# Kernel optimization log

Measured on AMD Instinct MI355X. Metric: run time of the kernel, lower is better.

## Reference

```python
import jax, jax.numpy as jnp
import numpy as np

B, N = 1, 768
CM, CP = 384, 128            # msa_channel (single repr), pair_channel
H, SQK, SV, PQK, PV = 12, 16, 16, 4, 8
NOUT = 384
NFIN = H * SV + H * PV * 4 + H * CP  # 2112
FP16_HUGE = 65504.0
DIST_EPS = 1e-8


def _quat_to_rot(q):
    # normalized quaternion [B,N,4] -> rotation matrix [B,N,3,3]
    q = q / jnp.sqrt(jnp.sum(q * q, axis=-1, keepdims=True))
    w, x, y, z = q[..., 0], q[..., 1], q[..., 2], q[..., 3]
    return jnp.stack([
        jnp.stack([1 - 2 * (y * y + z * z), 2 * (x * y - w * z), 2 * (x * z + w * y)], -1),
        jnp.stack([2 * (x * y + w * z), 1 - 2 * (x * x + z * z), 2 * (y * z - w * x)], -1),
        jnp.stack([2 * (x * z - w * y), 2 * (y * z + w * x), 1 - 2 * (x * x + y * y)], -1),
    ], -2)


def setup_inputs() -> dict:
    key = jax.random.key(0)
    ks = jax.random.split(key, 20)
    s = 0.02
    return {
        'inputs_1d': jax.random.normal(ks[0], (B, N, CM), jnp.float32),
        'inputs_2d': jax.random.normal(ks[1], (B, N, N, CP), jnp.float32),
        'mask': jnp.ones((B, N, 1), jnp.float32),
        'quat': jax.random.normal(ks[2], (B, N, 4), jnp.float32),
        'trans': jax.random.normal(ks[3], (B, N, 3), jnp.float32),
        'wq': jax.random.normal(ks[4], (CM, H * SQK), jnp.float32) * s,
        'bq': jnp.zeros((H * SQK,), jnp.float32),
        'wkv': jax.random.normal(ks[5], (CM, H * (SQK + SV)), jnp.float32) * s,
        'bkv': jnp.zeros((H * (SQK + SV),), jnp.float32),
        'wqp': jax.random.normal(ks[6], (CM, H * 3 * PQK), jnp.float32) * s,
        'bqp': jnp.zeros((H * 3 * PQK,), jnp.float32),
        'wkvp': jax.random.normal(ks[7], (CM, H * 3 * (PQK + PV)), jnp.float32) * s,
        'bkvp': jnp.zeros((H * 3 * (PQK + PV),), jnp.float32),
        'pw_raw': jnp.full((H,), 0.541323855, jnp.float32),
        'w2d': jax.random.normal(ks[8], (CP, H), jnp.float32) * s,
        'b2d': jnp.zeros((H,), jnp.float32),
        'wout': jax.random.normal(ks[9], (NFIN, NOUT), jnp.float32) * s,
        'bout': jnp.zeros((NOUT,), jnp.float32),
    }


def _ipa(inputs_1d, inputs_2d, mask, quat, trans,
         wq, bq, wkv, bkv, wqp, bqp, wkvp, bkvp, pw_raw, w2d, b2d, wout, bout):
    R = _quat_to_rot(quat)                      # [B,N,3,3]

    # --- scalar q/k/v ---
    q_s = (inputs_1d @ wq + bq).reshape(B, N, H, SQK)
    kv_s = (inputs_1d @ wkv + bkv).reshape(B, N, H, SQK + SV)
    k_s, v_s = kv_s[..., :SQK], kv_s[..., SQK:]

    # --- point q/k/v in global frame: R @ p_local + t ---
    qp = (inputs_1d @ wqp + bqp).reshape(B, N, 3, H * PQK)  # split order: x,y,z blocks
    qp_g = jnp.einsum('bnij,bnjp->bnip', R, qp) + trans[..., None]
    kvp = (inputs_1d @ wkvp + bkvp).reshape(B, N, 3, H * (PQK + PV))
    kvp_g = (jnp.einsum('bnij,bnjp->bnip', R, kvp) + trans[..., None]
             ).reshape(B, N, 3, H, PQK + PV)
    kp_g, vp_g = kvp_g[..., :PQK], kvp_g[..., PQK:]

    # --- attention weights ---
    scalar_w = (1.0 / (3.0 * SQK)) ** 0.5
    point_w = ((1.0 / (3.0 * PQK * 4.5)) ** 0.5) * jax.nn.softplus(pw_raw)  # [H]

    # point-distance logits: -0.5*w_h * sum_{xyz,p} (q-k)^2, via |q|^2+|k|^2-2qk
    q_pt = jnp.transpose(qp_g.reshape(B, N, 3, H, PQK), (0, 3, 1, 2, 4)).reshape(B, H, N, 3 * PQK)
    k_pt = jnp.transpose(kp_g, (0, 3, 1, 2, 4)).reshape(B, H, N, 3 * PQK)
    qq = jnp.sum(q_pt * q_pt, -1)               # [B,H,N]
    kk = jnp.sum(k_pt * k_pt, -1)
    cross = jnp.einsum('bhnd,bhmd->bhnm', q_pt, k_pt)
    attn_pt = -0.5 * point_w[None, :, None, None] * (
        qq[..., :, None] + kk[..., None, :] - 2.0 * cross)

    attn_sc = jnp.einsum('bnhd,bmhd->bhnm', q_s * scalar_w, k_s)
    a2d = jnp.transpose(inputs_2d @ w2d + b2d, (0, 3, 1, 2)) * (1.0 / 3.0) ** 0.5

    logits = attn_sc + attn_pt + a2d
    mask2d = mask * jnp.swapaxes(mask, -1, -2)  # [B,N,N]
    logits = logits - FP16_HUGE * (1.0 - mask2d[:, None])
    attn = jax.nn.softmax(logits, axis=-1)      # [B,H,N,N]

    # --- aggregation ---
    res_s = jnp.einsum('bhnm,bmhd->bnhd', attn, v_s).reshape(B, N, H * SV)
    v_pt = jnp.transpose(vp_g, (0, 3, 1, 2, 4)).reshape(B, H, N, 3 * PV)
    res_pt_g = jnp.einsum('bhnm,bhmd->bhnd', attn, v_pt).reshape(B, H, N, 3, PV)
    res_pt_g = jnp.transpose(res_pt_g, (0, 2, 3, 1, 4)).reshape(B, N, 3, H * PV)
    # invert point: R^T (g - t)
    res_pt_l = jnp.einsum('bnji,bnjp->bnip', R, res_pt_g - trans[..., None])  # [B,N,3,H*PV]
    pt_norm = jnp.sqrt(DIST_EPS + jnp.sum(res_pt_l * res_pt_l, axis=2))       # [B,N,H*PV]
    res_2d = jnp.einsum('bhnm,bnmc->bnhc', attn, inputs_2d).reshape(B, N, H * CP)

    final = jnp.concatenate(
        [res_s, res_pt_l[:, :, 0], res_pt_l[:, :, 1], res_pt_l[:, :, 2], pt_norm, res_2d], -1)
    return final @ wout + bout


def reference(inputs_1d, inputs_2d, mask, quat, trans,
              wq, bq, wkv, bkv, wqp, bqp, wkvp, bkvp, pw_raw, w2d, b2d, wout, bout):
    return _ipa(inputs_1d, inputs_2d, mask, quat, trans,
                wq, bq, wkv, bkv, wqp, bqp, wkvp, bkvp, pw_raw, w2d, b2d, wout, bout)
```

## Files before the change

### kernel.cpp

```cpp
#include <hip/hip_runtime.h>
#include <cstdint>
#include <cstddef>

static constexpr float SCALAR_W = 0.14433756729740643f;
static constexpr float PTW_C    = 0.13608276348795434f;
static constexpr float RSQRT3   = 0.5773502691896258f;
static constexpr float FP16HUGE = 65504.0f;

static constexpr size_t OFF_P    = 0;
static constexpr size_t OFF_R    = 884736;
static constexpr size_t OFF_QPG  = 891648;
static constexpr size_t OFF_KVPG = 1002240;
static constexpr size_t OFF_LG   = 1334016;
static constexpr size_t OFF_FIN  = 8633088;
static constexpr size_t OFF_VCAT = 10255104;
static constexpr size_t OFF_KST  = 10623744;
static constexpr size_t OFF_KPT  = 10771200;
static constexpr size_t WS_TOTAL = 10881792;

__global__ void k_sentinel(float* __restrict__ out, int nel, float val)
{
    const int i = blockIdx.x * 256 + threadIdx.x;
    if (i < nel) out[i] = val;
}

__global__ __launch_bounds__(256) void k_proj_all(const float* __restrict__ A,
    const float* __restrict__ wq,  const float* __restrict__ bq,
    const float* __restrict__ wkv, const float* __restrict__ bkv,
    const float* __restrict__ wqp, const float* __restrict__ bqp,
    const float* __restrict__ wkvp,const float* __restrict__ bkvp,
    float* __restrict__ P)
{
    const int z = blockIdx.z;
    const float* Bm; const float* bias; int ncols, colbase;
    switch (z) {
        case 0: Bm = wq;   bias = bq;   ncols = 192; colbase = 0;   break;
        case 1: Bm = wkv;  bias = bkv;  ncols = 384; colbase = 192; break;
        case 2: Bm = wqp;  bias = bqp;  ncols = 144; colbase = 576; break;
        default:Bm = wkvp; bias = bkvp; ncols = 432; colbase = 720; break;
    }
    if (blockIdx.x * 256 >= ncols) return;
    __shared__ float At[8][384];
    const int t = threadIdx.x;
    const int r0 = blockIdx.y * 8;
    const float4* A4 = reinterpret_cast<const float4*>(A + (size_t)r0 * 384);
    float4* At4 = reinterpret_cast<float4*>(&At[0][0]);
#pragma unroll
    for (int i = 0; i < 3; ++i) At4[t + 256 * i] = A4[t + 256 * i];
    __syncthreads();
    const int col = blockIdx.x * 256 + t;
    if (col >= ncols) return;
    float acc[8] = {0.f,0.f,0.f,0.f,0.f,0.f,0.f,0.f};
    const float* bp = Bm + col;
#pragma unroll 4
    for (int k = 0; k < 384; ++k) {
        const float b = bp[(size_t)k * ncols];
#pragma unroll
        for (int r = 0; r < 8; ++r) acc[r] += At[r][k] * b;
    }
    const float bb = bias[col];
#pragma unroll
    for (int r = 0; r < 8; ++r)
        P[(size_t)(r0 + r) * 1152 + colbase + col] = acc[r] + bb;
}

__global__ __launch_bounds__(256) void k_rmat(const float* __restrict__ quat,
    float* __restrict__ ws)
{
    const int o = blockIdx.x * 256 + threadIdx.x;
    if (o >= 768 * 9) return;
    const int n = o / 9, e = o - 9 * n;
    const float q0 = quat[n*4+0], q1 = quat[n*4+1], q2 = quat[n*4+2], q3 = quat[n*4+3];
    const float inv = 1.0f / sqrtf(q0*q0 + q1*q1 + q2*q2 + q3*q3);
    const float w = q0*inv, x = q1*inv, y = q2*inv, z = q3*inv;
    float R[9];
    R[0] = 1.f - 2.f*(y*y + z*z); R[1] = 2.f*(x*y - w*z); R[2] = 2.f*(x*z + w*y);
    R[3] = 2.f*(x*y + w*z); R[4] = 1.f - 2.f*(x*x + z*z); R[5] = 2.f*(y*z - w*x);
    R[6] = 2.f*(x*z - w*y); R[7] = 2.f*(y*z + w*x); R[8] = 1.f - 2.f*(x*x + y*y);
    ws[OFF_R + o] = R[e];
}

__global__ __launch_bounds__(256) void k_rigid(const float* __restrict__ trans,
    float* __restrict__ ws)
{
    const int o = blockIdx.x * 256 + threadIdx.x;
    if (o >= 768 * 576) return;
    const int n = o / 576, e = o - 576 * n;
    const float* R = ws + OFF_R + (size_t)n * 9;
    if (e < 144) {
        const int i = e / 48, p = e - 48 * i;
        const float* Pn = ws + OFF_P + (size_t)n * 1152 + 576;
        ws[OFF_QPG + (size_t)n*144 + e] =
            R[i*3+0]*Pn[p] + R[i*3+1]*Pn[48+p] + R[i*3+2]*Pn[96+p] + trans[n*3+i];
    } else {
        const int e2 = e - 144;
        const int i = e2 / 144, p = e2 - 144 * i;
        const float* Pn = ws + OFF_P + (size_t)n * 1152 + 720;
        ws[OFF_KVPG + (size_t)n*432 + e2] =
            R[i*3+0]*Pn[p] + R[i*3+1]*Pn[144+p] + R[i*3+2]*Pn[288+p] + trans[n*3+i];
    }
}

__global__ __launch_bounds__(256) void k_vcat(float* __restrict__ ws)
{
    const int o = blockIdx.x * 256 + threadIdx.x;
    if (o >= 768 * 480) return;
    const int m = o / 480, q = o - 480 * m;
    float v;
    if (q < 192) {
        const int h = q >> 4, d = q & 15;
        v = ws[OFF_P + (size_t)m*1152 + 192 + h*32 + 16 + d];
    } else {
        const int q2 = q - 192;
        const int i = q2 / 96, r = q2 - 96*i, h = r >> 3, c = r & 7;
        v = ws[OFF_KVPG + (size_t)m*432 + i*144 + h*12 + 4 + c];
    }
    ws[OFF_VCAT + o] = v;
}

__global__ __launch_bounds__(256) void k_kt(float* __restrict__ ws)
{
    const int o = blockIdx.x * 256 + threadIdx.x;
    if (o >= 768 * 336) return;
    const int m = o / 336, q = o - 336 * m;
    if (q < 192) {
        const int h = q >> 4, k = q & 15;
        ws[OFF_KST + (size_t)(h*16 + k)*768 + m] =
            ws[OFF_P + (size_t)m*1152 + 192 + h*32 + k];
    } else {
        const int d2 = q - 192;
        const int h = d2 / 12, d = d2 - 12 * h;
        const int i = d >> 2, a = d & 3;
        ws[OFF_KPT + (size_t)(h*12 + d)*768 + m] =
            ws[OFF_KVPG + (size_t)m*432 + i*144 + h*12 + a];
    }
}

__global__ __launch_bounds__(256) void k_lga(const float* __restrict__ in2d,
    const float* __restrict__ w2d, const float* __restrict__ b2d,
    const float* __restrict__ maskp, const float* __restrict__ pw_raw,
    float* __restrict__ ws)
{
    __shared__ float w2l[1536];
    __shared__ float a2l[12][132];
    __shared__ float qs[192], qpl[144], pwl[12], b2l[12];
    const int n = blockIdx.x, mt = blockIdx.y, t = threadIdx.x;
    if (t < 192) qs[t] = ws[OFF_P + (size_t)n*1152 + t] * SCALAR_W;
    if (t < 144) qpl[t] = ws[OFF_QPG + (size_t)n*144 + t];
    if (t < 12) {
        pwl[t] = PTW_C * logf(1.f + expf(pw_raw[t]));
        b2l[t] = b2d[t];
    }
    for (int i = t; i < 1536; i += 256) w2l[i] = w2d[i];
    const float mask_n = maskp[n];
    __syncthreads();

    const int cg = t & 3, pr = t >> 2;
#pragma unroll
    for (int half = 0; half < 2; ++half) {
        const int mm = half * 64 + pr;
        const int m = mt * 128 + mm;
        const float* p = in2d + ((size_t)n * 768 + m) * 128 + cg * 32;
        float acc[12] = {0,0,0,0,0,0,0,0,0,0,0,0};
#pragma unroll
        for (int cq = 0; cq < 8; ++cq) {
            const float4 v = *reinterpret_cast<const float4*>(p + cq * 4);
#pragma unroll
            for (int j = 0; j < 4; ++j) {
                const float x = (&v.x)[j];
                const int c = cg * 32 + cq * 4 + j;
#pragma unroll
                for (int h = 0; h < 12; ++h) acc[h] += x * w2l[c * 12 + h];
            }
        }
#pragma unroll
        for (int h = 0; h < 12; ++h) {
            acc[h] += __shfl_xor(acc[h], 1);
            acc[h] += __shfl_xor(acc[h], 2);
        }
        if (cg == 0) {
#pragma unroll
            for (int h = 0; h < 12; ++h)
                a2l[h][mm] = (acc[h] + b2l[h]) * RSQRT3;
        }
    }
    __syncthreads();

    const float* kst = ws + OFF_KST;
    const float* kpt = ws + OFF_KPT;
#pragma unroll
    for (int i = 0; i < 6; ++i) {
        const int idx = i * 256 + t;
        const int h = idx >> 7, mm = idx & 127;
        const int m = mt * 128 + mm;
        float sc = 0.f;
        const float* ks = kst + (size_t)(h*16)*768 + m;
#pragma unroll
        for (int k = 0; k < 16; ++k) sc += qs[h*16 + k] * ks[(size_t)k*768];
        float d2 = 0.f;
        const float* kp = kpt + (size_t)(h*12)*768 + m;
#pragma unroll
        for (int d = 0; d < 12; ++d) {
            const int ii = d >> 2, a = d & 3;
            const float dq = qpl[ii*48 + h*4 + a] - kp[(size_t)d*768];
            d2 += dq * dq;
        }
        const float pen = FP16HUGE * (1.f - mask_n * maskp[m]);
        ws[OFF_LG + ((size_t)n * 12 + h) * 768 + m] =
            sc - 0.5f * pwl[h] * d2 - pen + a2l[h][mm];
    }
}

__global__ __launch_bounds__(512) void k_att(const float* __restrict__ in2d,
    const float* __restrict__ trans, float* __restrict__ ws)
{
    __shared__ float at[12][776];
    __shared__ float fl[480];
    __shared__ float ptl[288];
    __shared__ float Rl[9], trl[3];
    const int n = blockIdx.x, t = threadIdx.x;
    const int wv = t >> 6, lane = t & 63;
    if (t < 9) Rl[t] = ws[OFF_R + n*9 + t];
    if (t < 3) trl[t] = trans[n*3 + t];
    {
        const float4* a4 = reinterpret_cast<const float4*>(ws + OFF_LG + (size_t)n * 9216);
        for (int i = t; i < 2304; i += 512) {
            const int row = i / 192, j = i - row * 192;
            *reinterpret_cast<float4*>(&at[row][j * 4]) = a4[i];
        }
    }
    __syncthreads();

    for (int h = wv; h < 12; h += 8) {
        float v[12];
        float mx = -3.0e38f;
#pragma unroll
        for (int i = 0; i < 12; ++i) { v[i] = at[h][lane + i*64]; mx = fmaxf(mx, v[i]); }
#pragma unroll
        for (int off = 32; off > 0; off >>= 1) mx = fmaxf(mx, __shfl_xor(mx, off));
        float s = 0.f;
#pragma unroll
        for (int i = 0; i < 12; ++i) { v[i] = expf(v[i] - mx); s += v[i]; }
#pragma unroll
        for (int off = 32; off > 0; off >>= 1) s += __shfl_xor(s, off);
        const float inv = 1.f / s;
#pragma unroll
        for (int i = 0; i < 12; ++i) at[h][lane + i*64] = v[i] * inv;
    }
    __syncthreads();

    {
        const int c = t & 127, g = t >> 7;
        const float* p = in2d + (size_t)n * 768 * 128 + c;
        float a0 = 0.f, a1 = 0.f, a2 = 0.f;
        for (int m = 0; m < 768; ++m) {
            const float x = p[(size_t)m * 128];
            a0 += at[g*3+0][m] * x;
            a1 += at[g*3+1][m] * x;
            a2 += at[g*3+2][m] * x;
        }
        float* fo = ws + OFF_FIN + (size_t)n * 2112 + 576;
        fo[(g*3+0)*128 + c] = a0;
        fo[(g*3+1)*128 + c] = a1;
        fo[(g*3+2)*128 + c] = a2;
    }

    if (t < 480) {
        int h;
        if (t < 192) h = t >> 4;
        else { const int r = (t - 192) % 96; h = r >> 3; }
        const float* v = ws + OFF_VCAT + t;
        const float* a = &at[h][0];
        float s = 0.f;
        for (int m = 0; m < 768; ++m) s += a[m] * v[(size_t)m * 480];
        fl[t] = s;
    }
    __syncthreads();

    float* fo = ws + OFF_FIN + (size_t)n * 2112;
    if (t < 192) fo[t] = fl[t];
    if (t < 288) {
        const int i = t / 96, p = t - 96 * i;
        float s = 0.f;
#pragma unroll
        for (int j = 0; j < 3; ++j)
            s += Rl[j*3 + i] * (fl[192 + j*96 + p] - trl[j]);
        fo[192 + t] = s;
        ptl[t] = s;
    }
    __syncthreads();
    if (t < 96) {
        const float a = ptl[t], b = ptl[96 + t], c = ptl[192 + t];
        fo[480 + t] = sqrtf(1e-8f + a*a + b*b + c*c);
    }
}

__global__ __launch_bounds__(256) void k_final(const float* __restrict__ wout,
    const float* __restrict__ bout, const float* __restrict__ ws,
    float* __restrict__ out)
{
    __shared__ float At[8][64];
    __shared__ float Bt[64][132];
    const float* fin = ws + OFF_FIN;
    const int r0 = blockIdx.y * 8;
    const int c0 = blockIdx.x * 128;
    const int t = threadIdx.x;
    const int c = t & 127, half = t >> 7;
    float acc[4] = {0.f, 0.f, 0.f, 0.f};
    for (int k0 = 0; k0 < 2112; k0 += 64) {
        __syncthreads();
        if (t < 128) {
            const int r = t >> 4, j = t & 15;
            *reinterpret_cast<float4*>(&At[r][j * 4]) =
                *reinterpret_cast<const float4*>(&fin[(size_t)(r0 + r) * 2112 + k0 + j * 4]);
        }
#pragma unroll
        for (int i = t; i < 2048; i += 256) {
            const int k = i >> 5, j = i & 31;
            *reinterpret_cast<float4*>(&Bt[k][j * 4]) =
                *reinterpret_cast<const float4*>(&wout[(size_t)(k0 + k) * 384 + c0 + j * 4]);
        }
        __syncthreads();
#pragma unroll
        for (int k = 0; k < 64; ++k) {
            const float b = Bt[k][c];
#pragma unroll
            for (int r = 0; r < 4; ++r) acc[r] += At[half*4 + r][k] * b;
        }
    }
#pragma unroll
    for (int r = 0; r < 4; ++r)
        out[(size_t)(r0 + half*4 + r) * 384 + c0 + c] = acc[r] + bout[c0 + c];
}

extern "C" void kernel_launch(void* const* d_in, const int* in_sizes, int n_in,
                              void* d_out, int out_size, void* d_ws, size_t ws_size,
                              hipStream_t stream)
{
    const float* in1d  = (const float*)d_in[0];
    const float* in2d  = (const float*)d_in[1];
    const float* maskp = (const float*)d_in[2];
    const float* quat  = (const float*)d_in[3];
    const float* trans = (const float*)d_in[4];
    const float* wq    = (const float*)d_in[5];
    const float* bq    = (const float*)d_in[6];
    const float* wkv   = (const float*)d_in[7];
    const float* bkv   = (const float*)d_in[8];
    const float* wqp   = (const float*)d_in[9];
    const float* bqp   = (const float*)d_in[10];
    const float* wkvp  = (const float*)d_in[11];
    const float* bkvp  = (const float*)d_in[12];
    const float* pwr   = (const float*)d_in[13];
    const float* w2d   = (const float*)d_in[14];
    const float* b2d   = (const float*)d_in[15];
    const float* wout  = (const float*)d_in[16];
    const float* bout  = (const float*)d_in[17];
    float* ws  = (float*)d_ws;
    float* out = (float*)d_out;

    if (ws_size < WS_TOTAL * sizeof(float)) {
        const float val = 1000.0f + (float)(ws_size / (1024.0 * 1024.0));
        k_sentinel<<<dim3((out_size + 255) / 256), dim3(256), 0, stream>>>(out, out_size, val);
        return;
    }

    dim3 blk(256);
    k_proj_all<<<dim3(2, 96, 4), blk, 0, stream>>>(in1d, wq, bq, wkv, bkv,
                                                   wqp, bqp, wkvp, bkvp, ws);
    k_rmat<<<dim3((768*9 + 255)/256), blk, 0, stream>>>(quat, ws);
    k_rigid<<<dim3((768*576 + 255)/256), blk, 0, stream>>>(trans, ws);
    k_vcat<<<dim3((768*480 + 255)/256), blk, 0, stream>>>(ws);
    k_kt<<<dim3((768*336 + 255)/256), blk, 0, stream>>>(ws);
    k_lga<<<dim3(768, 6), blk, 0, stream>>>(in2d, w2d, b2d, maskp, pwr, ws);
    k_att<<<dim3(768), dim3(512), 0, stream>>>(in2d, trans, ws);
    k_final<<<dim3(3, 96), blk, 0, stream>>>(wout, bout, ws, out);
}
```

Baseline: 525.6 us.

## Restructure pair-aggregation to split over m, merge layout kernels, widen logit tiles

The k_att pair-feature aggregation used to give each thread group all 768 rows for three heads. It now splits the m range across four groups, each accumulating all 12 heads, and reduces the partials through shared memory. Each in2d element is now loaded once per block instead of once per head group, which cuts global reads of the large pair tensor. k_vcat and k_kt are merged into a single launch, and k_lga now processes 256 m per block with one m per thread looping over heads, which also hoists the mask penalty out of the loop. The cost is extra shared memory (24KB of partials), more accumulator registers, and fewer k_lga blocks.

Result: slower. 536.5 us, median of 2 (+2.1%).

```diff
diff --git a/kernel.cpp b/kernel.cpp
--- a/kernel.cpp
+++ b/kernel.cpp
@@ -101,38 +101,36 @@
     }
 }
 
-__global__ __launch_bounds__(256) void k_vcat(float* __restrict__ ws)
+__global__ __launch_bounds__(256) void k_vk(float* __restrict__ ws)
 {
     const int o = blockIdx.x * 256 + threadIdx.x;
-    if (o >= 768 * 480) return;
-    const int m = o / 480, q = o - 480 * m;
-    float v;
-    if (q < 192) {
-        const int h = q >> 4, d = q & 15;
-        v = ws[OFF_P + (size_t)m*1152 + 192 + h*32 + 16 + d];
+    if (o < 768 * 480) {
+        const int m = o / 480, q = o - 480 * m;
+        float v;
+        if (q < 192) {
+            const int h = q >> 4, d = q & 15;
+            v = ws[OFF_P + (size_t)m*1152 + 192 + h*32 + 16 + d];
+        } else {
+            const int q2 = q - 192;
+            const int i = q2 / 96, r = q2 - 96*i, h = r >> 3, c = r & 7;
+            v = ws[OFF_KVPG + (size_t)m*432 + i*144 + h*12 + 4 + c];
+        }
+        ws[OFF_VCAT + o] = v;
     } else {
-        const int q2 = q - 192;
-        const int i = q2 / 96, r = q2 - 96*i, h = r >> 3, c = r & 7;
-        v = ws[OFF_KVPG + (size_t)m*432 + i*144 + h*12 + 4 + c];
-    }
-    ws[OFF_VCAT + o] = v;
-}
-
-__global__ __launch_bounds__(256) void k_kt(float* __restrict__ ws)
-{
-    const int o = blockIdx.x * 256 + threadIdx.x;
-    if (o >= 768 * 336) return;
-    const int m = o / 336, q = o - 336 * m;
-    if (q < 192) {
-        const int h = q >> 4, k = q & 15;
-        ws[OFF_KST + (size_t)(h*16 + k)*768 + m] =
-            ws[OFF_P + (size_t)m*1152 + 192 + h*32 + k];
-    } else {
-        const int d2 = q - 192;
-        const int h = d2 / 12, d = d2 - 12 * h;
-        const int i = d >> 2, a = d & 3;
-        ws[OFF_KPT + (size_t)(h*12 + d)*768 + m] =
-            ws[OFF_KVPG + (size_t)m*432 + i*144 + h*12 + a];
+        const int o2 = o - 768 * 480;
+        if (o2 >= 768 * 336) return;
+        const int m = o2 / 336, q = o2 - 336 * m;
+        if (q < 192) {
+            const int h = q >> 4, k = q & 15;
+            ws[OFF_KST + (size_t)(h*16 + k)*768 + m] =
+                ws[OFF_P + (size_t)m*1152 + 192 + h*32 + k];
+        } else {
+            const int d2 = q - 192;
+            const int h = d2 / 12, d = d2 - 12 * h;
+            const int i = d >> 2, a = d & 3;
+            ws[OFF_KPT + (size_t)(h*12 + d)*768 + m] =
+                ws[OFF_KVPG + (size_t)m*432 + i*144 + h*12 + a];
+        }
     }
 }
 
@@ -142,7 +140,7 @@
     float* __restrict__ ws)
 {
     __shared__ float w2l[1536];
-    __shared__ float a2l[12][132];
+    __shared__ float a2l[12][260];
     __shared__ float qs[192], qpl[144], pwl[12], b2l[12];
     const int n = blockIdx.x, mt = blockIdx.y, t = threadIdx.x;
     if (t < 192) qs[t] = ws[OFF_P + (size_t)n*1152 + t] * SCALAR_W;
@@ -157,9 +155,9 @@
 
     const int cg = t & 3, pr = t >> 2;
 #pragma unroll
-    for (int half = 0; half < 2; ++half) {
+    for (int half = 0; half < 4; ++half) {
         const int mm = half * 64 + pr;
-        const int m = mt * 128 + mm;
+        const int m = mt * 256 + mm;
         const float* p = in2d + ((size_t)n * 768 + m) * 128 + cg * 32;
         float acc[12] = {0,0,0,0,0,0,0,0,0,0,0,0};
 #pragma unroll
@@ -188,11 +186,10 @@
 
     const float* kst = ws + OFF_KST;
     const float* kpt = ws + OFF_KPT;
-#pragma unroll
-    for (int i = 0; i < 6; ++i) {
-        const int idx = i * 256 + t;
-        const int h = idx >> 7, mm = idx & 127;
-        const int m = mt * 128 + mm;
+    const int m = mt * 256 + t;
+    const float pen = FP16HUGE * (1.f - mask_n * maskp[m]);
+#pragma unroll
+    for (int h = 0; h < 12; ++h) {
         float sc = 0.f;
         const float* ks = kst + (size_t)(h*16)*768 + m;
 #pragma unroll
@@ -205,9 +202,8 @@
             const float dq = qpl[ii*48 + h*4 + a] - kp[(size_t)d*768];
             d2 += dq * dq;
         }
-        const float pen = FP16HUGE * (1.f - mask_n * maskp[m]);
         ws[OFF_LG + ((size_t)n * 12 + h) * 768 + m] =
-            sc - 0.5f * pwl[h] * d2 - pen + a2l[h][mm];
+            sc - 0.5f * pwl[h] * d2 - pen + a2l[h][t];
     }
 }
 
@@ -215,6 +211,7 @@
     const float* __restrict__ trans, float* __restrict__ ws)
 {
     __shared__ float at[12][776];
+    __shared__ float part[4][1536];
     __shared__ float fl[480];
     __shared__ float ptl[288];
     __shared__ float Rl[9], trl[3];
@@ -252,17 +249,22 @@
     {
         const int c = t & 127, g = t >> 7;
         const float* p = in2d + (size_t)n * 768 * 128 + c;
-        float a0 = 0.f, a1 = 0.f, a2 = 0.f;
-        for (int m = 0; m < 768; ++m) {
+        float acc[12] = {0,0,0,0,0,0,0,0,0,0,0,0};
+        const int m0 = g * 192;
+#pragma unroll 4
+        for (int m = m0; m < m0 + 192; ++m) {
             const float x = p[(size_t)m * 128];
-            a0 += at[g*3+0][m] * x;
-            a1 += at[g*3+1][m] * x;
-            a2 += at[g*3+2][m] * x;
-        }
+#pragma unroll
+            for (int h = 0; h < 12; ++h) acc[h] += at[h][m] * x;
+        }
+#pragma unroll
+        for (int h = 0; h < 12; ++h) part[g][h * 128 + c] = acc[h];
+    }
+    __syncthreads();
+    {
         float* fo = ws + OFF_FIN + (size_t)n * 2112 + 576;
-        fo[(g*3+0)*128 + c] = a0;
-        fo[(g*3+1)*128 + c] = a1;
-        fo[(g*3+2)*128 + c] = a2;
+        for (int o = t; o < 1536; o += 512)
+            fo[o] = part[0][o] + part[1][o] + part[2][o] + part[3][o];
     }
 
     if (t < 480) {
@@ -369,9 +371,8 @@
                                                    wqp, bqp, wkvp, bkvp, ws);
     k_rmat<<<dim3((768*9 + 255)/256), blk, 0, stream>>>(quat, ws);
     k_rigid<<<dim3((768*576 + 255)/256), blk, 0, stream>>>(trans, ws);
-    k_vcat<<<dim3((768*480 + 255)/256), blk, 0, stream>>>(ws);
-    k_kt<<<dim3((768*336 + 255)/256), blk, 0, stream>>>(ws);
-    k_lga<<<dim3(768, 6), blk, 0, stream>>>(in2d, w2d, b2d, maskp, pwr, ws);
+    k_vk<<<dim3((768*816 + 255)/256), blk, 0, stream>>>(ws);
+    k_lga<<<dim3(768, 3), blk, 0, stream>>>(in2d, w2d, b2d, maskp, pwr, ws);
     k_att<<<dim3(768), dim3(512), 0, stream>>>(in2d, trans, ws);
     k_final<<<dim3(3, 96), blk, 0, stream>>>(wout, bout, ws, out);
 }
```
